# Kernel tuning notes

Hardware: AMD Instinct MI355X
Metric: run time of the kernel (lower is better)

## Reference

```python
import jax, jax.numpy as jnp
import numpy as np

N = 100000
E = 3200000
IN_DIM, HID, MLP_HID, K = 3, 64, 128, 15


def setup_inputs() -> dict:
    key = jax.random.key(0)
    ks = jax.random.split(key, 10)
    x = jax.random.normal(ks[0], (N, IN_DIM), dtype=jnp.float32)
    edge_index = jax.random.randint(ks[1], (2, E), 0, N, dtype=jnp.int32)
    def glorot(k, shape):
        lim = float(np.sqrt(6.0 / (shape[0] + shape[1])))
        return jax.random.uniform(k, shape, jnp.float32, -lim, lim)
    return {
        "x": x,
        "edge_index": edge_index,
        "W1": glorot(ks[2], (IN_DIM, HID)), "b1": jnp.zeros((HID,), jnp.float32),
        "W2": glorot(ks[3], (HID, HID)),    "b2": jnp.zeros((HID,), jnp.float32),
        "Wm1": glorot(ks[4], (HID, MLP_HID)), "bm1": jnp.zeros((MLP_HID,), jnp.float32),
        "Wm2": glorot(ks[5], (MLP_HID, K)),   "bm2": jnp.zeros((K,), jnp.float32),
    }


def _gcn_layer(h, W, b, src, dst, deg_inv_sqrt, n):
    # h: [N, Fin] -> [N, Fout]; GCNConv: D^-1/2 (A+I) D^-1/2 (h W) + b
    hw = h @ W  # dense GEMM first (Fin small)
    norm = deg_inv_sqrt[src] * deg_inv_sqrt[dst]  # [E+N]
    msg = hw[src] * norm[:, None]                 # irregular gather, [E+N, Fout]
    out = jax.ops.segment_sum(msg, dst, num_segments=n)  # scatter-add
    return out + b


def reference(x, edge_index, W1, b1, W2, b2, Wm1, bm1, Wm2, bm2):
    n = x.shape[0]
    loops = jnp.arange(n, dtype=edge_index.dtype)
    src = jnp.concatenate([edge_index[0], loops])  # self-loops appended
    dst = jnp.concatenate([edge_index[1], loops])
    deg = jax.ops.segment_sum(jnp.ones_like(dst, dtype=x.dtype), dst, num_segments=n)
    deg_inv_sqrt = jnp.where(deg > 0, jax.lax.rsqrt(jnp.maximum(deg, 1.0)), 0.0)

    h = jax.nn.elu(_gcn_layer(x, W1, b1, src, dst, deg_inv_sqrt, n))
    h = jax.nn.elu(_gcn_layer(h, W2, b2, src, dst, deg_inv_sqrt, n))
    # MLP (dropout is identity in eval mode)
    h = jax.nn.elu(h @ Wm1 + bm1)
    H = h @ Wm2 + bm2
    return jax.nn.softmax(H, axis=1)  # [N, K]
```

## Files before the change

kernel.cpp:

```cpp
#include <hip/hip_runtime.h>
#include <hip/hip_fp16.h>
#include <math.h>


#define SPAN 128
#define CAP  6400
#define CH   8192
#define EPT  16
#define H2P  88
#define MSP2 136

typedef _Float16 v8hf __attribute__((ext_vector_type(8)));
typedef float    v4f  __attribute__((ext_vector_type(4)));

__device__ __forceinline__ float elu(float v) { return v > 0.f ? v : expm1f(v); }

__global__ __launch_bounds__(512) void scatter_kernel(const int* __restrict__ src,
    const int* __restrict__ dst, int* __restrict__ cursor, unsigned* __restrict__ colb,
    const float* __restrict__ W2, const float* __restrict__ Wm1,
    const float* __restrict__ Wm2, __half* __restrict__ W2t,
    __half* __restrict__ Wm1t, __half* __restrict__ Wm2p,
    __half* __restrict__ s1h, __half* __restrict__ sxh,
    int E, int NBK, int nChunks, int N) {
    int tid = threadIdx.x;
    if ((int)blockIdx.x == nChunks) {
        for (int i = tid; i < 64 * 64; i += 512) {
            int f = i >> 6, k = i & 63;
            W2t[f * 64 + k] = __float2half(W2[k * 64 + f]);
        }
        for (int i = tid; i < 128 * 64; i += 512) {
            int j = i >> 6, f = i & 63;
            Wm1t[j * 64 + f] = __float2half(Wm1[f * 128 + j]);
        }
        for (int i = tid; i < 4 * 64 * 8; i += 512) {
            int j = i & 7, l = (i >> 3) & 63, t = i >> 9;
            int k = t * 32 + (l >> 4) * 8 + j;
            int c = l & 15;
            Wm2p[i] = (c < 15) ? __float2half(Wm2[k * 15 + c]) : __half(0.f);
        }
        if (tid < 32) {
            ((uint2*)(s1h + (size_t)N * 64))[tid & 15] = uint2{0u, 0u};
            if (tid == 16) *((uint2*)(sxh + (size_t)N * 4)) = uint2{0u, 0u};
        }
        return;
    }
    __shared__ int hist[1024];
    __shared__ unsigned gb[1024];
    int chunk = blockIdx.x;
    for (int i = tid; i < NBK; i += 512) hist[i] = 0;
    __syncthreads();
    int base = chunk * CH;
    int cnt = min(CH, E - base);
    unsigned br[EPT], dt[EPT];
#pragma unroll
    for (int j = 0; j < EPT; ++j) {
        int idx = j * 512 + tid;
        br[j] = 0xFFFFFFFFu;
        if (idx < cnt) {
            int e = base + idx;
            int s = src[e], d = dst[e];
            int b = d >> 7;
            int r = atomicAdd(&hist[b], 1);
            br[j] = ((unsigned)b << 13) | (unsigned)r;
            dt[j] = ((unsigned)(d & 127) << 17) | (unsigned)s;
        }
    }
    __syncthreads();
    for (int b = tid; b < NBK; b += 512) {
        int c = hist[b];
        gb[b] = (unsigned)(b * CAP) + (c ? (unsigned)atomicAdd(&cursor[b], c) : 0u);
    }
    __syncthreads();
#pragma unroll
    for (int j = 0; j < EPT; ++j) {
        if (br[j] != 0xFFFFFFFFu) {
            int b = br[j] >> 13;
            int r = br[j] & 8191;
            unsigned pos = gb[b] + (unsigned)r;
            if (pos < (unsigned)(b + 1) * CAP) colb[pos] = dt[j];
        }
    }
}

__global__ __launch_bounds__(512) void csr_sort_kernel(unsigned* __restrict__ colb,
    const int* __restrict__ cursor, const float* __restrict__ x,
    uint2* __restrict__ rp2, float* __restrict__ dis, __half* __restrict__ sxh,
    int N) {
    __shared__ __align__(16) unsigned ebuf[CAP];
    __shared__ __align__(16) int sbuf[CAP];
    __shared__ int cnt[SPAN], pref[SPAN], fill[SPAN];
    int b = blockIdx.x, tid = threadIdx.x;
    int n = min(cursor[b], CAP);
    size_t base = (size_t)b * CAP;
    if (tid < SPAN) cnt[tid] = 0;
    int n4 = n >> 2;
    for (int k = tid; k < n4; k += 512)
        *(uint4*)(ebuf + 4 * k) = *(const uint4*)(colb + base + 4 * k);
    for (int i = (n4 << 2) + tid; i < n; i += 512) ebuf[i] = colb[base + i];
    __syncthreads();
    for (int i = tid; i < n; i += 512) atomicAdd(&cnt[(ebuf[i] >> 17) & 127], 1);
    __syncthreads();
    if (tid < 64) {
        int n0 = b * SPAN + tid;
        int n1 = n0 + 64;
        int s0 = (n0 < N) ? ((cnt[tid] + 16) & ~15) : 0;
        int s1 = (n1 < N) ? ((cnt[tid + 64] + 16) & ~15) : 0;
#pragma unroll
        for (int off = 1; off < 64; off <<= 1) {
            int t0 = __shfl_up(s0, off);
            int t1 = __shfl_up(s1, off);
            if (tid >= off) { s0 += t0; s1 += t1; }
        }
        int tot0 = __shfl(s0, 63);
        pref[tid] = s0;
        pref[tid + 64] = s1 + tot0;
    }
    __syncthreads();
    int ntot = pref[SPAN - 1];
    if (tid < SPAN) {
        int node = b * SPAN + tid;
        int c = cnt[tid];
        int pk = (node < N) ? ((c + 16) & ~15) : 0;
        int offP = pref[tid] - pk;
        fill[tid] = offP;
        if (node < N) {
            uint2 rp;
            rp.x = (unsigned)(base + offP);
            rp.y = (unsigned)(base + offP + c + 1);
            rp2[node] = rp;
            float r = rsqrtf((float)(c + 1));
            dis[node] = r;
            __half2 h0 = __floats2half2_rn(r * x[node * 3 + 0], r * x[node * 3 + 1]);
            __half2 h1 = __floats2half2_rn(r * x[node * 3 + 2], 0.f);
            uint2 w; w.x = *(unsigned*)&h0; w.y = *(unsigned*)&h1;
            *(uint2*)(sxh + (size_t)node * 4) = w;
            sbuf[offP + c] = node;
            for (int j = c + 1; j < pk; ++j) sbuf[offP + j] = N;
        }
    }
    __syncthreads();
    for (int i = tid; i < n; i += 512) {
        unsigned e = ebuf[i];
        int pos = atomicAdd(&fill[(e >> 17) & 127], 1);
        sbuf[pos] = (int)(e & 0x1FFFF);
    }
    __syncthreads();
    int nt4 = (ntot + 3) >> 2;
    for (int k = tid; k < nt4; k += 512)
        *(uint4*)(colb + base + 4 * k) = *(const uint4*)(sbuf + 4 * k);
}

__global__ void agg3_kernel(const __half* __restrict__ sxh, const uint2* __restrict__ rp2,
                            const unsigned* __restrict__ colb, const float* __restrict__ dis,
                            const float* __restrict__ W1, const float* __restrict__ b1,
                            __half* __restrict__ s1h, int N) {
    int wave = (blockIdx.x * blockDim.x + threadIdx.x) >> 6;
    int lane = threadIdx.x & 63;
    int hl = lane & 31;
    int d = wave * 2 + (lane >> 5);
    bool act = d < N;
    int start = 0, end = 0;
    if (act) { uint2 rp = rp2[d]; start = (int)rp.x; end = (int)rp.y; }
    float a0 = 0.f, a1 = 0.f, a2v = 0.f;
    for (int i = start + hl; i < end; i += 32) {
        uint2 rq = *(const uint2*)(sxh + (size_t)colb[i] * 4);
        float2 u0 = __half22float2(*(__half2*)&rq.x);
        float2 u1 = __half22float2(*(__half2*)&rq.y);
        a0 += u0.x; a1 += u0.y; a2v += u1.x;
    }
#pragma unroll
    for (int off = 16; off; off >>= 1) {
        a0  += __shfl_xor(a0, off);
        a1  += __shfl_xor(a1, off);
        a2v += __shfl_xor(a2v, off);
    }
    if (act) {
        float r = dis[d];
        float v0 = r * (a0 * W1[hl]      + a1 * W1[64 + hl]      + a2v * W1[128 + hl])      + b1[hl];
        float v1 = r * (a0 * W1[32 + hl] + a1 * W1[96 + hl]      + a2v * W1[160 + hl])      + b1[32 + hl];
        s1h[(size_t)d * 64 + hl]      = __float2half(r * elu(v0));
        s1h[(size_t)d * 64 + 32 + hl] = __float2half(r * elu(v1));
    }
}

__global__ void agg64_kernel(const __half* __restrict__ s1h, const uint2* __restrict__ rp2,
                             const unsigned* __restrict__ colb, const float* __restrict__ dis,
                             __half* __restrict__ a2h, int N) {
    int wave = (blockIdx.x * blockDim.x + threadIdx.x) >> 6;
    int lane = threadIdx.x & 63;
    int g = lane >> 3;
    int f = lane & 7;
    int d = wave;
    if (d >= N) return;
    uint2 rp = rp2[d];
    float r = dis[d];
    int start = (int)rp.x;
    int len = (int)(rp.y - rp.x);
    int pend = start + ((len + 15) & ~15);
    float acc0 = 0.f, acc1 = 0.f, acc2 = 0.f, acc3 = 0.f;
    float acc4 = 0.f, acc5 = 0.f, acc6 = 0.f, acc7 = 0.f;
    for (int i = start; i < pend; i += 16) {
        int ca = (int)colb[i + g];
        int cb = (int)colb[i + 8 + g];
        uint4 A = *(const uint4*)(s1h + (size_t)ca * 64 + f * 8);
        uint4 B = *(const uint4*)(s1h + (size_t)cb * 64 + f * 8);
        __half2 p0 = __hadd2(*(__half2*)&A.x, *(__half2*)&B.x);
        __half2 p1 = __hadd2(*(__half2*)&A.y, *(__half2*)&B.y);
        __half2 p2 = __hadd2(*(__half2*)&A.z, *(__half2*)&B.z);
        __half2 p3 = __hadd2(*(__half2*)&A.w, *(__half2*)&B.w);
        float2 q0 = __half22float2(p0);
        float2 q1 = __half22float2(p1);
        float2 q2 = __half22float2(p2);
        float2 q3 = __half22float2(p3);
        acc0 += q0.x; acc1 += q0.y; acc2 += q1.x; acc3 += q1.y;
        acc4 += q2.x; acc5 += q2.y; acc6 += q3.x; acc7 += q3.y;
    }
#pragma unroll
    for (int off = 8; off <= 32; off <<= 1) {
        acc0 += __shfl_xor(acc0, off);
        acc1 += __shfl_xor(acc1, off);
        acc2 += __shfl_xor(acc2, off);
        acc3 += __shfl_xor(acc3, off);
        acc4 += __shfl_xor(acc4, off);
        acc5 += __shfl_xor(acc5, off);
        acc6 += __shfl_xor(acc6, off);
        acc7 += __shfl_xor(acc7, off);
    }
    if (g == 0) {
        __half2 o0 = __floats2half2_rn(r * acc0, r * acc1);
        __half2 o1 = __floats2half2_rn(r * acc2, r * acc3);
        __half2 o2 = __floats2half2_rn(r * acc4, r * acc5);
        __half2 o3 = __floats2half2_rn(r * acc6, r * acc7);
        uint4 w;
        w.x = *(unsigned*)&o0; w.y = *(unsigned*)&o1;
        w.z = *(unsigned*)&o2; w.w = *(unsigned*)&o3;
        *(uint4*)(a2h + (size_t)d * 64 + f * 8) = w;
    }
}

__global__ __launch_bounds__(256) void h1_kernel(const __half* __restrict__ a2h,
    const __half* __restrict__ W2t, const float* __restrict__ b2g,
    const __half* __restrict__ Wm1t, const float* __restrict__ bm1g,
    const __half* __restrict__ Wm2p, const float* __restrict__ bm2g,
    float* __restrict__ out, int N) {
    __shared__ __align__(16) __half h2s[64 * H2P];
    __shared__ __align__(16) __half ms[64 * MSP2];
    int tid = threadIdx.x;
    int wave = tid >> 6, lane = tid & 63;
    int q = lane >> 4, l16 = lane & 15;
    int base = blockIdx.x * 64;

    v8hf wc[4];
#pragma unroll
    for (int t = 0; t < 4; ++t)
        wc[t] = *(const v8hf*)(Wm2p + ((size_t)(t * 64 + lane)) * 8);
    float bbc = (l16 < 15) ? bm2g[l16] : 0.f;

    {
        int nodeRow = base + wave * 16 + l16;
        size_t arow = (size_t)min(nodeRow, N - 1) * 64;
        v8hf af0 = *(const v8hf*)(a2h + arow + q * 8);
        v8hf af1 = *(const v8hf*)(a2h + arow + 32 + q * 8);
#pragma unroll
        for (int fb = 0; fb < 4; ++fb) {
            float bb = b2g[fb * 16 + l16];
            v4f acc = {bb, bb, bb, bb};
            v8hf b0 = *(const v8hf*)(W2t + (fb * 16 + l16) * 64 + q * 8);
            v8hf b1 = *(const v8hf*)(W2t + (fb * 16 + l16) * 64 + 32 + q * 8);
            acc = __builtin_amdgcn_mfma_f32_16x16x32_f16(af0, b0, acc, 0, 0, 0);
            acc = __builtin_amdgcn_mfma_f32_16x16x32_f16(af1, b1, acc, 0, 0, 0);
#pragma unroll
            for (int r = 0; r < 4; ++r)
                h2s[(wave * 16 + q * 4 + r) * H2P + fb * 16 + l16] =
                    __float2half(elu(acc[r]));
        }
    }
    __syncthreads();
    {
        int arow = (wave * 16 + l16) * H2P;
        v8hf af0 = *(const v8hf*)(h2s + arow + q * 8);
        v8hf af1 = *(const v8hf*)(h2s + arow + 32 + q * 8);
#pragma unroll
        for (int jb = 0; jb < 8; ++jb) {
            float bb = bm1g[jb * 16 + l16];
            v4f acc = {bb, bb, bb, bb};
            v8hf b0 = *(const v8hf*)(Wm1t + (jb * 16 + l16) * 64 + q * 8);
            v8hf b1 = *(const v8hf*)(Wm1t + (jb * 16 + l16) * 64 + 32 + q * 8);
            acc = __builtin_amdgcn_mfma_f32_16x16x32_f16(af0, b0, acc, 0, 0, 0);
            acc = __builtin_amdgcn_mfma_f32_16x16x32_f16(af1, b1, acc, 0, 0, 0);
#pragma unroll
            for (int r = 0; r < 4; ++r)
                ms[(wave * 16 + q * 4 + r) * MSP2 + jb * 16 + l16] =
                    __float2half(elu(acc[r]));
        }
    }
    __syncthreads();
    {
        int arow = (wave * 16 + l16) * MSP2;
        v4f accC = {bbc, bbc, bbc, bbc};
#pragma unroll
        for (int t = 0; t < 4; ++t) {
            v8hf a = *(const v8hf*)(ms + arow + t * 32 + q * 8);
            accC = __builtin_amdgcn_mfma_f32_16x16x32_f16(a, wc[t], accC, 0, 0, 0);
        }
#pragma unroll
        for (int r = 0; r < 4; ++r) {
            float lg = (l16 < 15) ? accC[r] : -1e30f;
            float mx = lg;
            mx = fmaxf(mx, __shfl_xor(mx, 1));
            mx = fmaxf(mx, __shfl_xor(mx, 2));
            mx = fmaxf(mx, __shfl_xor(mx, 4));
            mx = fmaxf(mx, __shfl_xor(mx, 8));
            float ex = (l16 < 15) ? __expf(lg - mx) : 0.f;
            float sden = ex;
            sden += __shfl_xor(sden, 1);
            sden += __shfl_xor(sden, 2);
            sden += __shfl_xor(sden, 4);
            sden += __shfl_xor(sden, 8);
            int node = base + wave * 16 + q * 4 + r;
            if (l16 < 15 && node < N)
                out[(size_t)node * 15 + l16] = ex / sden;
        }
    }
}

extern "C" void kernel_launch(void* const* d_in, const int* in_sizes, int n_in,
                              void* d_out, int out_size, void* d_ws, size_t ws_size,
                              hipStream_t stream) {
    const float* x   = (const float*)d_in[0];
    const int*   ei  = (const int*)d_in[1];
    const float* W1  = (const float*)d_in[2];
    const float* b1  = (const float*)d_in[3];
    const float* W2  = (const float*)d_in[4];
    const float* b2  = (const float*)d_in[5];
    const float* Wm1 = (const float*)d_in[6];
    const float* bm1 = (const float*)d_in[7];
    const float* Wm2 = (const float*)d_in[8];
    const float* bm2 = (const float*)d_in[9];
    float* out = (float*)d_out;

    int N = in_sizes[0] / 3;
    int E = in_sizes[1] / 2;
    const int* src = ei;
    const int* dst = ei + E;
    int NBK = (N + SPAN - 1) / SPAN;

    uintptr_t p = (uintptr_t)d_ws;
    auto carve = [&](size_t bytes) -> void* {
        p = (p + 255) & ~(uintptr_t)255;
        void* r = (void*)p;
        p += bytes;
        return r;
    };
    unsigned* colb    = (unsigned*)carve((size_t)NBK * CAP * 4 + 256);
    __half*   a2h     = (__half*)carve((size_t)N * 64 * 2);
    __half*   s1h     = (__half*)carve((size_t)(N + 1) * 64 * 2);
    int*      cursor  = (int*)carve((size_t)NBK * 4);
    uint2*    rp2     = (uint2*)carve((size_t)N * 8);
    float*    dis     = (float*)carve((size_t)N * 4);
    __half*   sxh     = (__half*)carve((size_t)(N + 1) * 8);
    __half*   W2t     = (__half*)carve(64 * 64 * 2);
    __half*   Wm1t    = (__half*)carve(128 * 64 * 2);
    __half*   Wm2p    = (__half*)carve(4 * 64 * 8 * 2);

    int nChunks = (E + CH - 1) / CH;
    int aggBlocks = (N + 7) / 8;
    int aggBlocks64 = (N + 3) / 4;
    int nTiles = (N + 63) / 64;

    hipMemsetAsync(cursor, 0, (size_t)NBK * 4, stream);
    scatter_kernel<<<nChunks + 1, 512, 0, stream>>>(src, dst, cursor, colb,
        W2, Wm1, Wm2, W2t, Wm1t, Wm2p, s1h, sxh, E, NBK, nChunks, N);
    csr_sort_kernel<<<NBK, 512, 0, stream>>>(colb, cursor, x, rp2, dis, sxh, N);
    agg3_kernel<<<aggBlocks, 256, 0, stream>>>(sxh, rp2, colb, dis, W1, b1, s1h, N);
    agg64_kernel<<<aggBlocks64, 256, 0, stream>>>(s1h, rp2, colb, dis, a2h, N);
    h1_kernel<<<nTiles, 256, 0, stream>>>(a2h, W2t, b2, Wm1t, bm1, Wm2p, bm2, out, N);
}
```

Measured before the change: 234.8 us.

## Replace bucketed scatter+LDS sort CSR build with global count/scan/place atomics

Replaces the two-pass bucket scatter and per-bucket shared-memory counting sort with three kernels: a global atomic degree count, a per-bucket scan that writes row pointers and self-loop padding, and a place pass that atomically claims slots per destination node. This drops the intermediate packed buffer and the LDS sort, at the cost of 3.2M scattered global atomics on per-node counters twice. Column order within a row becomes nondeterministic.

```diff
diff --git a/kernel.cpp b/kernel.cpp
--- a/kernel.cpp
+++ b/kernel.cpp
@@ -5,8 +5,6 @@
 
 #define SPAN 128
 #define CAP  6400
-#define CH   8192
-#define EPT  16
 #define H2P  88
 #define MSP2 136
 
@@ -15,15 +13,15 @@
 
 __device__ __forceinline__ float elu(float v) { return v > 0.f ? v : expm1f(v); }
 
-__global__ __launch_bounds__(512) void scatter_kernel(const int* __restrict__ src,
-    const int* __restrict__ dst, int* __restrict__ cursor, unsigned* __restrict__ colb,
+__global__ __launch_bounds__(512) void count_kernel(const int* __restrict__ dst,
+    int* __restrict__ deg,
     const float* __restrict__ W2, const float* __restrict__ Wm1,
     const float* __restrict__ Wm2, __half* __restrict__ W2t,
     __half* __restrict__ Wm1t, __half* __restrict__ Wm2p,
     __half* __restrict__ s1h, __half* __restrict__ sxh,
-    int E, int NBK, int nChunks, int N) {
+    int E, int nCB, int N) {
     int tid = threadIdx.x;
-    if ((int)blockIdx.x == nChunks) {
+    if ((int)blockIdx.x == nCB) {
         for (int i = tid; i < 64 * 64; i += 512) {
             int f = i >> 6, k = i & 63;
             W2t[f * 64 + k] = __float2half(W2[k * 64 + f]);
@@ -44,110 +42,64 @@
         }
         return;
     }
-    __shared__ int hist[1024];
-    __shared__ unsigned gb[1024];
-    int chunk = blockIdx.x;
-    for (int i = tid; i < NBK; i += 512) hist[i] = 0;
-    __syncthreads();
-    int base = chunk * CH;
-    int cnt = min(CH, E - base);
-    unsigned br[EPT], dt[EPT];
-#pragma unroll
-    for (int j = 0; j < EPT; ++j) {
-        int idx = j * 512 + tid;
-        br[j] = 0xFFFFFFFFu;
-        if (idx < cnt) {
-            int e = base + idx;
-            int s = src[e], d = dst[e];
-            int b = d >> 7;
-            int r = atomicAdd(&hist[b], 1);
-            br[j] = ((unsigned)b << 13) | (unsigned)r;
-            dt[j] = ((unsigned)(d & 127) << 17) | (unsigned)s;
-        }
-    }
-    __syncthreads();
-    for (int b = tid; b < NBK; b += 512) {
-        int c = hist[b];
-        gb[b] = (unsigned)(b * CAP) + (c ? (unsigned)atomicAdd(&cursor[b], c) : 0u);
-    }
-    __syncthreads();
-#pragma unroll
-    for (int j = 0; j < EPT; ++j) {
-        if (br[j] != 0xFFFFFFFFu) {
-            int b = br[j] >> 13;
-            int r = br[j] & 8191;
-            unsigned pos = gb[b] + (unsigned)r;
-            if (pos < (unsigned)(b + 1) * CAP) colb[pos] = dt[j];
-        }
-    }
-}
-
-__global__ __launch_bounds__(512) void csr_sort_kernel(unsigned* __restrict__ colb,
-    const int* __restrict__ cursor, const float* __restrict__ x,
-    uint2* __restrict__ rp2, float* __restrict__ dis, __half* __restrict__ sxh,
+    int stride = nCB * 512;
+    for (int e = blockIdx.x * 512 + tid; e < E; e += stride)
+        atomicAdd(&deg[dst[e]], 1);
+}
+
+__global__ __launch_bounds__(64) void build_kernel(const int* __restrict__ deg,
+    const float* __restrict__ x, int* __restrict__ fill, uint2* __restrict__ rp2,
+    float* __restrict__ dis, __half* __restrict__ sxh, unsigned* __restrict__ colb,
     int N) {
-    __shared__ __align__(16) unsigned ebuf[CAP];
-    __shared__ __align__(16) int sbuf[CAP];
-    __shared__ int cnt[SPAN], pref[SPAN], fill[SPAN];
-    int b = blockIdx.x, tid = threadIdx.x;
-    int n = min(cursor[b], CAP);
-    size_t base = (size_t)b * CAP;
-    if (tid < SPAN) cnt[tid] = 0;
-    int n4 = n >> 2;
-    for (int k = tid; k < n4; k += 512)
-        *(uint4*)(ebuf + 4 * k) = *(const uint4*)(colb + base + 4 * k);
-    for (int i = (n4 << 2) + tid; i < n; i += 512) ebuf[i] = colb[base + i];
-    __syncthreads();
-    for (int i = tid; i < n; i += 512) atomicAdd(&cnt[(ebuf[i] >> 17) & 127], 1);
-    __syncthreads();
-    if (tid < 64) {
-        int n0 = b * SPAN + tid;
-        int n1 = n0 + 64;
-        int s0 = (n0 < N) ? ((cnt[tid] + 16) & ~15) : 0;
-        int s1 = (n1 < N) ? ((cnt[tid + 64] + 16) & ~15) : 0;
-#pragma unroll
-        for (int off = 1; off < 64; off <<= 1) {
-            int t0 = __shfl_up(s0, off);
-            int t1 = __shfl_up(s1, off);
-            if (tid >= off) { s0 += t0; s1 += t1; }
-        }
-        int tot0 = __shfl(s0, 63);
-        pref[tid] = s0;
-        pref[tid + 64] = s1 + tot0;
-    }
-    __syncthreads();
-    int ntot = pref[SPAN - 1];
-    if (tid < SPAN) {
-        int node = b * SPAN + tid;
-        int c = cnt[tid];
-        int pk = (node < N) ? ((c + 16) & ~15) : 0;
-        int offP = pref[tid] - pk;
-        fill[tid] = offP;
+    int b = blockIdx.x, t = threadIdx.x;
+    int n0 = b * SPAN + t, n1 = n0 + 64;
+    int c0 = (n0 < N) ? deg[n0] : 0;
+    int c1 = (n1 < N) ? deg[n1] : 0;
+    int p0 = (n0 < N) ? ((c0 + 16) & ~15) : 0;
+    int p1 = (n1 < N) ? ((c1 + 16) & ~15) : 0;
+    int s0 = p0, s1 = p1;
+#pragma unroll
+    for (int off = 1; off < 64; off <<= 1) {
+        int t0 = __shfl_up(s0, off);
+        int t1 = __shfl_up(s1, off);
+        if (t >= off) { s0 += t0; s1 += t1; }
+    }
+    int tot0 = __shfl(s0, 63);
+    unsigned base = (unsigned)b * CAP;
+    unsigned st0 = base + (unsigned)(s0 - p0);
+    unsigned st1 = base + (unsigned)(tot0 + s1 - p1);
+#pragma unroll
+    for (int hv = 0; hv < 2; ++hv) {
+        int node = hv ? n1 : n0;
+        int c    = hv ? c1 : c0;
+        int pk   = hv ? p1 : p0;
+        unsigned start = hv ? st1 : st0;
         if (node < N) {
-            uint2 rp;
-            rp.x = (unsigned)(base + offP);
-            rp.y = (unsigned)(base + offP + c + 1);
+            uint2 rp; rp.x = start; rp.y = start + (unsigned)c + 1u;
             rp2[node] = rp;
+            fill[node] = (int)start;
             float r = rsqrtf((float)(c + 1));
             dis[node] = r;
             __half2 h0 = __floats2half2_rn(r * x[node * 3 + 0], r * x[node * 3 + 1]);
             __half2 h1 = __floats2half2_rn(r * x[node * 3 + 2], 0.f);
             uint2 w; w.x = *(unsigned*)&h0; w.y = *(unsigned*)&h1;
             *(uint2*)(sxh + (size_t)node * 4) = w;
-            sbuf[offP + c] = node;
-            for (int j = c + 1; j < pk; ++j) sbuf[offP + j] = N;
-        }
-    }
-    __syncthreads();
-    for (int i = tid; i < n; i += 512) {
-        unsigned e = ebuf[i];
-        int pos = atomicAdd(&fill[(e >> 17) & 127], 1);
-        sbuf[pos] = (int)(e & 0x1FFFF);
-    }
-    __syncthreads();
-    int nt4 = (ntot + 3) >> 2;
-    for (int k = tid; k < nt4; k += 512)
-        *(uint4*)(colb + base + 4 * k) = *(const uint4*)(sbuf + 4 * k);
+            colb[start + c] = (unsigned)node;
+            for (int j = c + 1; j < pk; ++j) colb[start + j] = (unsigned)N;
+        }
+    }
+}
+
+__global__ __launch_bounds__(512) void place_kernel(const int* __restrict__ src,
+    const int* __restrict__ dst, int* __restrict__ fill, unsigned* __restrict__ colb,
+    int E, int nPB) {
+    int stride = nPB * 512;
+    for (int e = blockIdx.x * 512 + threadIdx.x; e < E; e += stride) {
+        int s = src[e], d = dst[e];
+        unsigned pos = (unsigned)atomicAdd(&fill[d], 1);
+        unsigned lim = ((unsigned)(d >> 7) + 1u) * CAP;
+        if (pos < lim) colb[pos] = (unsigned)s;
+    }
 }
 
 __global__ void agg3_kernel(const __half* __restrict__ sxh, const uint2* __restrict__ rp2,
@@ -355,7 +307,8 @@
     unsigned* colb    = (unsigned*)carve((size_t)NBK * CAP * 4 + 256);
     __half*   a2h     = (__half*)carve((size_t)N * 64 * 2);
     __half*   s1h     = (__half*)carve((size_t)(N + 1) * 64 * 2);
-    int*      cursor  = (int*)carve((size_t)NBK * 4);
+    int*      fill    = (int*)carve((size_t)N * 4);
+    int*      deg     = (int*)carve((size_t)N * 4);
     uint2*    rp2     = (uint2*)carve((size_t)N * 8);
     float*    dis     = (float*)carve((size_t)N * 4);
     __half*   sxh     = (__half*)carve((size_t)(N + 1) * 8);
@@ -363,15 +316,17 @@
     __half*   Wm1t    = (__half*)carve(128 * 64 * 2);
     __half*   Wm2p    = (__half*)carve(4 * 64 * 8 * 2);
 
-    int nChunks = (E + CH - 1) / CH;
+    int nCB = 782;
+    int nPB = 782;
     int aggBlocks = (N + 7) / 8;
     int aggBlocks64 = (N + 3) / 4;
     int nTiles = (N + 63) / 64;
 
-    hipMemsetAsync(cursor, 0, (size_t)NBK * 4, stream);
-    scatter_kernel<<<nChunks + 1, 512, 0, stream>>>(src, dst, cursor, colb,
-        W2, Wm1, Wm2, W2t, Wm1t, Wm2p, s1h, sxh, E, NBK, nChunks, N);
-    csr_sort_kernel<<<NBK, 512, 0, stream>>>(colb, cursor, x, rp2, dis, sxh, N);
+    hipMemsetAsync(deg, 0, (size_t)N * 4, stream);
+    count_kernel<<<nCB + 1, 512, 0, stream>>>(dst, deg,
+        W2, Wm1, Wm2, W2t, Wm1t, Wm2p, s1h, sxh, E, nCB, N);
+    build_kernel<<<NBK, 64, 0, stream>>>(deg, x, fill, rp2, dis, sxh, colb, N);
+    place_kernel<<<nPB, 512, 0, stream>>>(src, dst, fill, colb, E, nPB);
     agg3_kernel<<<aggBlocks, 256, 0, stream>>>(sxh, rp2, colb, dis, W1, b1, s1h, N);
     agg64_kernel<<<aggBlocks64, 256, 0, stream>>>(s1h, rp2, colb, dis, a2h, N);
     h1_kernel<<<nTiles, 256, 0, stream>>>(a2h, W2t, b2, Wm1t, bm1, Wm2p, bm2, out, N);
```

After: 592.2 us. 152% more time.
